# Kernel tuning notes

Hardware: AMD Instinct MI355X
Metric: run time of the kernel (lower is better)

Reference implementation:

```python
import jax, jax.numpy as jnp
import numpy as np

STRIDE = (2, 2)  # from init_kwargs


def setup_inputs() -> dict:
    key = jax.random.key(0)
    kx, kw_, kb = jax.random.split(key, 3)
    x = jax.random.normal(kx, (8, 256, 64, 64), dtype=jnp.float32)
    weight = jax.random.normal(kw_, (128, 256, 4, 4), dtype=jnp.float32) * 0.02
    bias = jax.random.normal(kb, (128, 4, 4), dtype=jnp.float32) * 0.01
    return {"x": x, "weight": weight, "bias": bias}


def reference(x, weight, bias):
    # x: (b, i, h, w); weight: (o, i, kh, kw); bias: (o, kh, kw)
    b, c, h, w = x.shape
    o, _, kh, kw = weight.shape
    sh, sw = STRIDE
    # Outer-product contraction: (b, o, kh, kw, h, w)
    y = jnp.einsum('bihw,oixy->boxyhw', x, weight)
    # Bias is added per kernel position BEFORE the overlap-add fold,
    # so overlapping output pixels accumulate multiple bias copies
    # (faithful to the original module).
    y = y + bias[None, :, :, :, None, None]
    nh = (h - 1) * sh + kh
    nw = (w - 1) * sw + kw
    out = jnp.zeros((b, o, nh, nw), dtype=x.dtype)
    # fold: overlap-add scatter over the kh*kw kernel positions (small fixed loop)
    for ky in range(kh):
        for kxp in range(kw):
            out = out.at[:, :,
                         ky:ky + (h - 1) * sh + 1:sh,
                         kxp:kxp + (w - 1) * sw + 1:sw].add(y[:, :, ky, kxp])
    return out
```

## Files before the change

### kernel.cpp

```cpp
#include <hip/hip_runtime.h>
#include <stdint.h>
#include <stddef.h>

#define GLOBAL_AS __attribute__((address_space(1)))
#define LDS_AS    __attribute__((address_space(3)))

typedef __bf16 bf16x8 __attribute__((ext_vector_type(8)));
typedef float  f32x4  __attribute__((ext_vector_type(4)));

constexpr int NB = 8, CI = 256, H_ = 64, W_ = 64, CO = 128;
constexpr int OH = 130, OW = 130;
constexpr int PU = 65;
constexpr int PAD = 66;
constexpr int NPIX = PU * PU;
constexpr int NTOT = NB * NPIX;
constexpr int NT_N = 265;

constexpr size_t XPAD_BYTES = (size_t)NB * PAD * PAD * CI * 2;
constexpr size_t A_OFF      = XPAD_BYTES;
constexpr size_t A_BYTES    = (size_t)512 * 1024 * 2;
constexpr size_t B_OFF      = A_OFF + A_BYTES;

__device__ __forceinline__ void gload_lds16(const void* g, void* l) {
  __builtin_amdgcn_global_load_lds((GLOBAL_AS void*)g, (LDS_AS void*)l, 16, 0, 0);
}

__global__ void prep_x(const float* __restrict__ x, __bf16* __restrict__ xp) {
  __shared__ float tile[64][65];
  const int h   = blockIdx.x;
  const int bat = blockIdx.y;
  const int t   = threadIdx.x;
  if (h >= 64) {
    const int row = (h == 64) ? 0 : 65;
    __bf16* dst = xp + (size_t)(bat * PAD + row) * PAD * CI;
    bf16x8 z = {};
    for (int idx = t; idx < PAD * CI / 8; idx += 256)
      *(bf16x8*)(dst + (size_t)idx * 8) = z;
    return;
  }
  if (t < 64) {
    __bf16* rowp = xp + (size_t)(bat * PAD + h + 1) * PAD * CI;
    bf16x8 z = {};
    int half = t >> 5, part = t & 31;
    *(bf16x8*)(rowp + (size_t)half * 65 * CI + part * 8) = z;
  }
  for (int ch = 0; ch < 4; ++ch) {
    const int i0 = ch * 64;
    const float* src = x + (((size_t)(bat * CI + i0)) * H_ + h) * W_;
    if (ch) __syncthreads();
#pragma unroll
    for (int r = 0; r < 4; ++r) {
      int ii = r * 16 + (t >> 4);
      int ww = (t & 15) * 4;
      float4 v = *(const float4*)(src + (size_t)ii * H_ * W_ + ww);
      tile[ii][ww] = v.x; tile[ii][ww + 1] = v.y; tile[ii][ww + 2] = v.z; tile[ii][ww + 3] = v.w;
    }
    __syncthreads();
    __bf16* dst = xp + ((size_t)(bat * PAD + h + 1) * PAD + 1) * CI + i0;
#pragma unroll
    for (int r = 0; r < 2; ++r) {
      int s  = r * 256 + t;
      int ww = s >> 3;
      int ig = (s & 7) * 8;
      bf16x8 o;
#pragma unroll
      for (int k = 0; k < 8; ++k) o[k] = (__bf16)tile[ig + k][ww];
      *(bf16x8*)(dst + (size_t)ww * CI + ig) = o;
    }
  }
}

__global__ void build_ab(const float* __restrict__ w, const __bf16* __restrict__ xp,
                         __bf16* __restrict__ amat, __bf16* __restrict__ bmat) {
  const int bid = blockIdx.x;
  const int t   = threadIdx.x;
  if (bid < 16900) {
    const int g = bid * 256 + t;
    const int n = g >> 7, c = g & 127;
    const int tap = c >> 5, ic = c & 31;
    const int a = tap >> 1, cc = tap & 1;
    const int bat = n / NPIX, pr = n % NPIX;
    const int u = pr / PU, v = pr % PU;
    const __bf16* src = xp + (((size_t)(bat * PAD + u + 1 - a)) * PAD + (v + 1 - cc)) * CI + ic * 8;
    *(bf16x8*)(bmat + (size_t)n * 1024 + (size_t)c * 8) = *(const bf16x8*)src;
  } else {
    const int tid = (bid - 16900) * 256 + t;
    const int i   = tid & 255;
    const int tap = (tid >> 8) & 3;
    const int row = (tid >> 10) & 255;
    const int py  = tid >> 18;
    const int a = tap >> 1, c = tap & 1;
    const int o = row >> 1, px = row & 1;
    amat[tid] = (__bf16)w[(size_t)(o * CI + i) * 16 + (py + 2 * a) * 4 + (px + 2 * c)];
  }
}

__global__ __launch_bounds__(256) void deconv_mfma(
    const __bf16* __restrict__ amat, const __bf16* __restrict__ bmat,
    const float* __restrict__ bias, float* __restrict__ out) {
  const int wg   = blockIdx.x;
  const int mt_i = wg & 3;
  const int nt_i = wg >> 2;
  const int nBase = nt_i * 128;

  __shared__ alignas(16) __bf16 lds[2][8192];

  const int t    = threadIdx.x;
  const int wid  = t >> 6, lane = t & 63;
  const int lr   = lane & 15, kg = lane >> 4;
  const int wr   = wid >> 1, wc = wid & 1;

  const int m0   = t >> 2;
  const int kst  = (t & 3) ^ ((m0 >> 1) & 3);
  const __bf16* srcA  = amat + ((size_t)(mt_i * 128 + m0)) * 1024 + kst * 8;
  int nA = nBase + m0;       if (nA > NTOT - 1) nA = NTOT - 1;
  int nB2 = nBase + m0 + 64; if (nB2 > NTOT - 1) nB2 = NTOT - 1;
  const __bf16* srcB  = bmat + (size_t)nA  * 1024 + kst * 8;
  const __bf16* srcB2 = bmat + (size_t)nB2 * 1024 + kst * 8;

  const int swz = (lr >> 1) & 3;
  int offA[4], offB[4];
#pragma unroll
  for (int mt = 0; mt < 4; ++mt)
    offA[mt] = (wr * 64 + mt * 16 + lr) * 32 + ((kg ^ swz) * 8);
#pragma unroll
  for (int nt = 0; nt < 4; ++nt)
    offB[nt] = 4096 + (wc * 64 + nt * 16 + lr) * 32 + ((kg ^ swz) * 8);

  f32x4 acc[4][4] = {};

  auto stage = [&](int buf, int s) {
    const size_t ko = (size_t)s * 32;
    __bf16* l = &lds[buf][0];
    gload_lds16(srcA  + ko,              l + (size_t)t * 8);
    gload_lds16(srcA  + 64 * 1024 + ko,  l + (size_t)t * 8 + 2048);
    gload_lds16(srcB  + ko,              l + 4096 + (size_t)t * 8);
    gload_lds16(srcB2 + ko,              l + 4096 + (size_t)t * 8 + 2048);
  };

  stage(0, 0);
  __syncthreads();
  int cur = 0;
  for (int s = 0; s < 32; ++s) {
    if (s < 31) stage(cur ^ 1, s + 1);
    const __bf16* base = &lds[cur][0];
    bf16x8 af[4], bfr[4];
#pragma unroll
    for (int mt = 0; mt < 4; ++mt) af[mt]  = *(const bf16x8*)(base + offA[mt]);
#pragma unroll
    for (int nt = 0; nt < 4; ++nt) bfr[nt] = *(const bf16x8*)(base + offB[nt]);
#pragma unroll
    for (int mt = 0; mt < 4; ++mt)
#pragma unroll
      for (int nt = 0; nt < 4; ++nt)
        acc[mt][nt] = __builtin_amdgcn_mfma_f32_16x16x32_bf16(af[mt], bfr[nt], acc[mt][nt], 0, 0, 0);
    __syncthreads();
    cur ^= 1;
  }

  const int py = mt_i >> 1;
#pragma unroll
  for (int mt = 0; mt < 4; ++mt) {
    const int rbase = (mt_i & 1) * 128 + wr * 64 + mt * 16 + kg * 4;
    const int o0 = rbase >> 1, o1 = o0 + 1;
#pragma unroll
    for (int nt = 0; nt < 4; ++nt) {
      const int n = nBase + wc * 64 + nt * 16 + lr;
      if (n < NTOT) {
        const int bat = n / NPIX, pr = n % NPIX;
        const int u = pr / PU, v = pr % PU;
        const int oy = 2 * u + py;
        const bool a0 = (u <= 63), a1 = (u >= 1);
        const bool c0 = (v <= 63), c1 = (v >= 1);
        auto bs = [&](int o, int px) {
          const float* bp = bias + (size_t)o * 16;
          float s0 = 0.f;
          if (a0 && c0) s0 += bp[py * 4 + px];
          if (a0 && c1) s0 += bp[py * 4 + px + 2];
          if (a1 && c0) s0 += bp[(py + 2) * 4 + px];
          if (a1 && c1) s0 += bp[(py + 2) * 4 + px + 2];
          return s0;
        };
        const size_t b0 = ((size_t)(bat * CO + o0) * OH + oy) * OW + 2 * v;
        const size_t b1 = ((size_t)(bat * CO + o1) * OH + oy) * OW + 2 * v;
        float2 w0, w1;
        w0.x = acc[mt][nt][0] + bs(o0, 0);
        w0.y = acc[mt][nt][1] + bs(o0, 1);
        w1.x = acc[mt][nt][2] + bs(o1, 0);
        w1.y = acc[mt][nt][3] + bs(o1, 1);
        *(float2*)(out + b0) = w0;
        *(float2*)(out + b1) = w1;
      }
    }
  }
}

extern "C" void kernel_launch(void* const* d_in, const int* in_sizes, int n_in,
                              void* d_out, int out_size, void* d_ws, size_t ws_size,
                              hipStream_t stream) {
  const float* x    = (const float*)d_in[0];
  const float* w    = (const float*)d_in[1];
  const float* bias = (const float*)d_in[2];
  float* out = (float*)d_out;
  char* ws = (char*)d_ws;
  __bf16* xpad = (__bf16*)ws;
  __bf16* amat = (__bf16*)(ws + A_OFF);
  __bf16* bmat = (__bf16*)(ws + B_OFF);

  prep_x<<<dim3(66, 8), 256, 0, stream>>>(x, xpad);
  build_ab<<<dim3(16900 + 2048), 256, 0, stream>>>(w, xpad, amat, bmat);
  deconv_mfma<<<dim3(4 * NT_N), 256, 0, stream>>>(amat, bmat, bias, out);
}
```

Before: 203.4 us.

## Gather B implicitly from padded input and enlarge GEMM tile with interleaved pipeline

Drops the explicit im2col B matrix and reads tap-shifted rows of the padded bf16 input directly into LDS. Weight repacking moves to a small dedicated kernel. The GEMM now uses a 256x256 tile with 512 threads and 128KB of LDS, over a fine-grained schedule that interleaves loads, barriers and MFMA with set-priority hints. This removes a large intermediate write and read and raises per-block data reuse, at the cost of lower occupancy and many extra barriers.

```diff
diff --git a/kernel.cpp b/kernel.cpp
--- a/kernel.cpp
+++ b/kernel.cpp
@@ -14,12 +14,10 @@
 constexpr int PAD = 66;
 constexpr int NPIX = PU * PU;
 constexpr int NTOT = NB * NPIX;
-constexpr int NT_N = 265;
+constexpr int NT_N = 133;
 
 constexpr size_t XPAD_BYTES = (size_t)NB * PAD * PAD * CI * 2;
 constexpr size_t A_OFF      = XPAD_BYTES;
-constexpr size_t A_BYTES    = (size_t)512 * 1024 * 2;
-constexpr size_t B_OFF      = A_OFF + A_BYTES;
 
 __device__ __forceinline__ void gload_lds16(const void* g, void* l) {
   __builtin_amdgcn_global_load_lds((GLOBAL_AS void*)g, (LDS_AS void*)l, 16, 0, 0);
@@ -70,102 +68,137 @@
   }
 }
 
-__global__ void build_ab(const float* __restrict__ w, const __bf16* __restrict__ xp,
-                         __bf16* __restrict__ amat, __bf16* __restrict__ bmat) {
-  const int bid = blockIdx.x;
-  const int t   = threadIdx.x;
-  if (bid < 16900) {
-    const int g = bid * 256 + t;
-    const int n = g >> 7, c = g & 127;
-    const int tap = c >> 5, ic = c & 31;
-    const int a = tap >> 1, cc = tap & 1;
-    const int bat = n / NPIX, pr = n % NPIX;
-    const int u = pr / PU, v = pr % PU;
-    const __bf16* src = xp + (((size_t)(bat * PAD + u + 1 - a)) * PAD + (v + 1 - cc)) * CI + ic * 8;
-    *(bf16x8*)(bmat + (size_t)n * 1024 + (size_t)c * 8) = *(const bf16x8*)src;
-  } else {
-    const int tid = (bid - 16900) * 256 + t;
-    const int i   = tid & 255;
-    const int tap = (tid >> 8) & 3;
-    const int row = (tid >> 10) & 255;
-    const int py  = tid >> 18;
-    const int a = tap >> 1, c = tap & 1;
-    const int o = row >> 1, px = row & 1;
-    amat[tid] = (__bf16)w[(size_t)(o * CI + i) * 16 + (py + 2 * a) * 4 + (px + 2 * c)];
-  }
-}
-
-__global__ __launch_bounds__(256) void deconv_mfma(
-    const __bf16* __restrict__ amat, const __bf16* __restrict__ bmat,
+__global__ void prep_w3(const float* __restrict__ w, __bf16* __restrict__ amat) {
+  const int o = blockIdx.x, t = threadIdx.x;
+  const float* src = w + (size_t)o * 4096 + t * 16;
+  float4 v0 = *(const float4*)(src);
+  float4 v1 = *(const float4*)(src + 4);
+  float4 v2 = *(const float4*)(src + 8);
+  float4 v3 = *(const float4*)(src + 12);
+  float vals[16] = {v0.x, v0.y, v0.z, v0.w, v1.x, v1.y, v1.z, v1.w,
+                    v2.x, v2.y, v2.z, v2.w, v3.x, v3.y, v3.z, v3.w};
+#pragma unroll
+  for (int ky = 0; ky < 4; ++ky)
+#pragma unroll
+    for (int kx = 0; kx < 4; ++kx) {
+      const int pyy = ky & 1, a = ky >> 1, pxx = kx & 1, c = kx >> 1;
+      amat[((size_t)(pyy * 256 + o * 2 + pxx)) * 1024 + (a * 2 + c) * 256 + t] =
+          (__bf16)vals[ky * 4 + kx];
+    }
+}
+
+__global__ __launch_bounds__(512, 2) void deconv_mfma(
+    const __bf16* __restrict__ xp, const __bf16* __restrict__ amat,
     const float* __restrict__ bias, float* __restrict__ out) {
-  const int wg   = blockIdx.x;
-  const int mt_i = wg & 3;
-  const int nt_i = wg >> 2;
-  const int nBase = nt_i * 128;
-
-  __shared__ alignas(16) __bf16 lds[2][8192];
+  const int wg    = blockIdx.x;
+  const int py    = wg / NT_N;
+  const int nt_i  = wg % NT_N;
+  const int nBase = nt_i * 256;
+
+  __shared__ char ldsc[131072] __attribute__((aligned(16)));
 
   const int t    = threadIdx.x;
   const int wid  = t >> 6, lane = t & 63;
   const int lr   = lane & 15, kg = lane >> 4;
-  const int wr   = wid >> 1, wc = wid & 1;
-
-  const int m0   = t >> 2;
-  const int kst  = (t & 3) ^ ((m0 >> 1) & 3);
-  const __bf16* srcA  = amat + ((size_t)(mt_i * 128 + m0)) * 1024 + kst * 8;
-  int nA = nBase + m0;       if (nA > NTOT - 1) nA = NTOT - 1;
-  int nB2 = nBase + m0 + 64; if (nB2 > NTOT - 1) nB2 = NTOT - 1;
-  const __bf16* srcB  = bmat + (size_t)nA  * 1024 + kst * 8;
-  const __bf16* srcB2 = bmat + (size_t)nB2 * 1024 + kst * 8;
-
-  const int swz = (lr >> 1) & 3;
-  int offA[4], offB[4];
-#pragma unroll
-  for (int mt = 0; mt < 4; ++mt)
-    offA[mt] = (wr * 64 + mt * 16 + lr) * 32 + ((kg ^ swz) * 8);
-#pragma unroll
-  for (int nt = 0; nt < 4; ++nt)
-    offB[nt] = 4096 + (wc * 64 + nt * 16 + lr) * 32 + ((kg ^ swz) * 8);
-
-  f32x4 acc[4][4] = {};
-
-  auto stage = [&](int buf, int s) {
-    const size_t ko = (size_t)s * 32;
-    __bf16* l = &lds[buf][0];
-    gload_lds16(srcA  + ko,              l + (size_t)t * 8);
-    gload_lds16(srcA  + 64 * 1024 + ko,  l + (size_t)t * 8 + 2048);
-    gload_lds16(srcB  + ko,              l + 4096 + (size_t)t * 8);
-    gload_lds16(srcB2 + ko,              l + 4096 + (size_t)t * 8 + 2048);
-  };
-
-  stage(0, 0);
-  __syncthreads();
-  int cur = 0;
-  for (int s = 0; s < 32; ++s) {
-    if (s < 31) stage(cur ^ 1, s + 1);
-    const __bf16* base = &lds[cur][0];
-    bf16x8 af[4], bfr[4];
-#pragma unroll
-    for (int mt = 0; mt < 4; ++mt) af[mt]  = *(const bf16x8*)(base + offA[mt]);
-#pragma unroll
-    for (int nt = 0; nt < 4; ++nt) bfr[nt] = *(const bf16x8*)(base + offB[nt]);
-#pragma unroll
-    for (int mt = 0; mt < 4; ++mt)
-#pragma unroll
-      for (int nt = 0; nt < 4; ++nt)
-        acc[mt][nt] = __builtin_amdgcn_mfma_f32_16x16x32_bf16(af[mt], bfr[nt], acc[mt][nt], 0, 0, 0);
-    __syncthreads();
-    cur ^= 1;
-  }
-
-  const int py = mt_i >> 1;
-#pragma unroll
-  for (int mt = 0; mt < 4; ++mt) {
-    const int rbase = (mt_i & 1) * 128 + wr * 64 + mt * 16 + kg * 4;
+  const int wm   = wid >> 2, wn = wid & 3;
+
+  const int r0 = t >> 3;
+  const int gA = (t & 7) ^ (r0 & 7);
+  const __bf16* srcA_t = amat + ((size_t)(py * 256 + r0)) * 1024 + gA * 8;
+  int obB[2][2];
+#pragma unroll
+  for (int h = 0; h < 2; ++h)
+#pragma unroll
+    for (int j = 0; j < 2; ++j) {
+      int n = nBase + h * 128 + r0 + 64 * j;
+      if (n > NTOT - 1) n = NTOT - 1;
+      const int bat = n / NPIX, pr = n % NPIX;
+      const int u = pr / PU, v = pr % PU;
+      obB[h][j] = ((bat * PAD + u + 1) * PAD + (v + 1)) * CI + gA * 8;
+    }
+
+  const int xorA0 = (kg ^ (lr & 7)) * 16;
+  const int rowA  = (wm * 128 + lr) * 128;
+  const int rowB  = 32768 + (wn * 64 + lr) * 128;
+
+  f32x4 acc[8][4] = {};
+  bf16x8 af[8][2], bf[4][2];
+
+#define HSA(buf, tile, h) do {                                                  \
+    char* _l = ldsc + (buf) * 65536 + (h) * 16384 + t * 16;                     \
+    const __bf16* _s = srcA_t + (size_t)((h) * 128) * 1024 + (tile) * 64;       \
+    gload_lds16(_s, _l);                                                        \
+    gload_lds16(_s + 64 * 1024, _l + 8192);                                     \
+  } while (0)
+
+#define HSB(buf, tile, h) do {                                                  \
+    char* _l = ldsc + (buf) * 65536 + 32768 + (h) * 16384 + t * 16;             \
+    const int _off = ((tile) & 3) * 64 - (((tile) >> 3) * PAD + (((tile) >> 2) & 1)) * CI; \
+    gload_lds16(xp + obB[h][0] + _off, _l);                                     \
+    gload_lds16(xp + obB[h][1] + _off, _l + 8192);                              \
+  } while (0)
+
+#define RDA(buf, mtb) do {                                                      \
+    _Pragma("unroll")                                                           \
+    for (int _q = 0; _q < 4; ++_q) {                                            \
+      af[(mtb) + _q][0] = *(const bf16x8*)(ldsc + (buf) * 65536 + rowA + ((mtb) + _q) * 2048 + xorA0);        \
+      af[(mtb) + _q][1] = *(const bf16x8*)(ldsc + (buf) * 65536 + rowA + ((mtb) + _q) * 2048 + (xorA0 ^ 64)); \
+    }                                                                           \
+  } while (0)
+
+#define RDB(buf, ntb) do {                                                      \
+    _Pragma("unroll")                                                           \
+    for (int _q = 0; _q < 2; ++_q) {                                            \
+      bf[(ntb) + _q][0] = *(const bf16x8*)(ldsc + (buf) * 65536 + rowB + ((ntb) + _q) * 2048 + xorA0);        \
+      bf[(ntb) + _q][1] = *(const bf16x8*)(ldsc + (buf) * 65536 + rowB + ((ntb) + _q) * 2048 + (xorA0 ^ 64)); \
+    }                                                                           \
+  } while (0)
+
+#define MM(qm, qn) do {                                                         \
+    __builtin_amdgcn_s_setprio(1);                                              \
+    _Pragma("unroll")                                                           \
+    for (int _a = 0; _a < 4; ++_a)                                              \
+      _Pragma("unroll")                                                         \
+      for (int _b = 0; _b < 2; ++_b) {                                          \
+        acc[(qm)*4+_a][(qn)*2+_b] = __builtin_amdgcn_mfma_f32_16x16x32_bf16(    \
+            af[(qm)*4+_a][0], bf[(qn)*2+_b][0], acc[(qm)*4+_a][(qn)*2+_b], 0, 0, 0); \
+        acc[(qm)*4+_a][(qn)*2+_b] = __builtin_amdgcn_mfma_f32_16x16x32_bf16(    \
+            af[(qm)*4+_a][1], bf[(qn)*2+_b][1], acc[(qm)*4+_a][(qn)*2+_b], 0, 0, 0); \
+      }                                                                         \
+    __builtin_amdgcn_s_setprio(0);                                              \
+  } while (0)
+
+#define BAR __builtin_amdgcn_s_barrier()
+#define WAITV(n) asm volatile("s_waitcnt vmcnt(" #n ")" ::: "memory")
+
+  HSA(0, 0, 0); HSA(0, 0, 1); HSB(0, 0, 0); HSB(0, 0, 1);
+  HSA(1, 1, 0); HSA(1, 1, 1);
+  WAITV(4);
+  BAR;
+
+#pragma unroll 1
+  for (int i = 0; i < 8; ++i) {
+    const int T1 = 2 * i + 1, P0 = 2 * i + 2, P1 = 2 * i + 3;
+    const bool last = (i == 7);
+     RDA(0, 0); RDB(0, 0); HSB(1, T1, 0); BAR; MM(0, 0); BAR;
+     RDA(0, 4); RDB(0, 2); HSB(1, T1, 1); BAR; MM(1, 1); BAR;
+     if (!last) HSA(0, P0, 0); BAR; MM(0, 1); BAR;
+     if (!last) { HSA(0, P0, 1); WAITV(4); } else { WAITV(0); }
+            BAR; MM(1, 0); BAR;
+     RDA(1, 0); RDB(1, 0); if (!last) HSB(0, P0, 0); BAR; MM(0, 0); BAR;
+     RDA(1, 4); RDB(1, 2); if (!last) HSB(0, P0, 1); BAR; MM(1, 1); BAR;
+     if (!last) HSA(1, P1, 0); BAR; MM(0, 1); BAR;
+     if (!last) { HSA(1, P1, 1); WAITV(4); }
+            BAR; MM(1, 0); BAR;
+  }
+
+#pragma unroll
+  for (int mt = 0; mt < 8; ++mt) {
+    const int rbase = wm * 128 + mt * 16 + kg * 4;
     const int o0 = rbase >> 1, o1 = o0 + 1;
 #pragma unroll
     for (int nt = 0; nt < 4; ++nt) {
-      const int n = nBase + wc * 64 + nt * 16 + lr;
+      const int n = nBase + wn * 64 + nt * 16 + lr;
       if (n < NTOT) {
         const int bat = n / NPIX, pr = n % NPIX;
         const int u = pr / PU, v = pr % PU;
@@ -193,6 +226,13 @@
       }
     }
   }
+#undef HSA
+#undef HSB
+#undef RDA
+#undef RDB
+#undef MM
+#undef BAR
+#undef WAITV
 }
 
 extern "C" void kernel_launch(void* const* d_in, const int* in_sizes, int n_in,
@@ -205,9 +245,8 @@
   char* ws = (char*)d_ws;
   __bf16* xpad = (__bf16*)ws;
   __bf16* amat = (__bf16*)(ws + A_OFF);
-  __bf16* bmat = (__bf16*)(ws + B_OFF);
 
   prep_x<<<dim3(66, 8), 256, 0, stream>>>(x, xpad);
-  build_ab<<<dim3(16900 + 2048), 256, 0, stream>>>(w, xpad, amat, bmat);
-  deconv_mfma<<<dim3(4 * NT_N), 256, 0, stream>>>(amat, bmat, bias, out);
-}
+  prep_w3<<<dim3(128), 256, 0, stream>>>(w, amat);
+  deconv_mfma<<<dim3(2 * NT_N), 512, 0, stream>>>(xpad, amat, bias, out);
+}
```

Result: slower. 225.2 us (+10.7%).
